# Kernel tuning notes

Measured on AMD Instinct MI355X. Metric: run time of the kernel, lower is better.

Reference implementation:

```python
import jax, jax.numpy as jnp
import numpy as np

N, E = 50000, 500000
IN_C, HID, OUT_C, HEADS, NL = 128, 16, 16, 8, 4
EPS = 1e-5
NEG_SLOPE = 0.2


def _gatv2(x, src, dst, Wl, Wr, att, bias, concat):
    # GATv2Conv (PyG semantics, eval mode): lin_l on source, lin_r on target,
    # e = a . LeakyReLU(xl[src] + xr[dst]); segment softmax over dst; scatter-sum.
    n = x.shape[0]
    H, C = att.shape
    xl = (x @ Wl).reshape(n, H, C)
    xr = (x @ Wr).reshape(n, H, C)
    e = jax.nn.leaky_relu(xl[src] + xr[dst], NEG_SLOPE)          # [E', H, C]
    logit = jnp.einsum('ehc,hc->eh', e, att)                      # [E', H]
    mx = jax.lax.stop_gradient(jax.ops.segment_max(logit, dst, num_segments=n))
    a = jnp.exp(logit - mx[dst])
    denom = jax.ops.segment_sum(a, dst, num_segments=n)
    alpha = a / denom[dst]                                        # [E', H]
    out = jax.ops.segment_sum(xl[src] * alpha[..., None], dst, num_segments=n)
    out = out.reshape(n, H * C) if concat else out.mean(axis=1)
    return out + bias


def _bn_eval(x, g, b, m, v):
    return (x - m) * jax.lax.rsqrt(v + EPS) * g + b


def setup_inputs() -> dict:
    key = jax.random.key(0)
    ks = jax.random.split(key, 32)
    d = {}
    d['x'] = jax.random.normal(ks[0], (N, IN_C), dtype=jnp.float32)
    d['edge_index'] = jax.random.randint(ks[1], (2, E), 0, N, dtype=jnp.int64)
    HC = HID * HEADS  # 128
    dims_in = [IN_C, HC, HC, HC]
    dims_h = [HEADS, HEADS, HEADS, 1]
    dims_c = [HID, HID, HID, OUT_C]
    ki = 2
    for i in range(NL):
        fan = dims_in[i]
        s = 1.0 / np.sqrt(fan)
        d[f'W{i}l'] = jax.random.uniform(ks[ki], (fan, dims_h[i] * dims_c[i]), minval=-s, maxval=s, dtype=jnp.float32); ki += 1
        d[f'W{i}r'] = jax.random.uniform(ks[ki], (fan, dims_h[i] * dims_c[i]), minval=-s, maxval=s, dtype=jnp.float32); ki += 1
        d[f'a{i}'] = jax.random.normal(ks[ki], (dims_h[i], dims_c[i]), dtype=jnp.float32) * 0.1; ki += 1
        out_dim = dims_h[i] * dims_c[i] if i < NL - 1 else dims_c[i]
        d[f'b{i}'] = jnp.zeros((out_dim,), dtype=jnp.float32)
    for i in range(NL - 1):
        d[f'g{i}'] = jnp.ones((HC,), dtype=jnp.float32) + 0.1 * jax.random.normal(ks[ki], (HC,), dtype=jnp.float32); ki += 1
        d[f'be{i}'] = 0.1 * jax.random.normal(ks[ki], (HC,), dtype=jnp.float32); ki += 1
        d[f'm{i}'] = 0.1 * jax.random.normal(ks[ki], (HC,), dtype=jnp.float32); ki += 1
        d[f'v{i}'] = jnp.ones((HC,), dtype=jnp.float32)
    return d


def reference(x, edge_index, W0l, W0r, a0, b0, W1l, W1r, a1, b1, W2l, W2r, a2, b2, W3l, W3r, a3, b3, g0, be0, m0, v0, g1, be1, m1, v1, g2, be2, m2, v2):
    n = x.shape[0]
    loop = jnp.arange(n, dtype=edge_index.dtype)
    src = jnp.concatenate([edge_index[0], loop])  # add_self_loops=True (PyG default)
    dst = jnp.concatenate([edge_index[1], loop])
    Ws = [(W0l, W0r, a0, b0), (W1l, W1r, a1, b1), (W2l, W2r, a2, b2), (W3l, W3r, a3, b3)]
    bns = [(g0, be0, m0, v0), (g1, be1, m1, v1), (g2, be2, m2, v2)]
    h = x
    for i in range(NL):
        Wl, Wr, att, bias = Ws[i]
        h = _gatv2(h, src, dst, Wl, Wr, att, bias, concat=(i < NL - 1))
        if i < NL - 1:
            g, b, m, v = bns[i]
            h = jax.nn.elu(_bn_eval(h, g, b, m, v))
    return h
```

## Files before the change

kernel.cpp:

```cpp
#include <hip/hip_runtime.h>
#include <hip/hip_fp16.h>
#include <math.h>

static constexpr float BN_EPS = 1e-5f;
static constexpr float NEG = 0.2f;

typedef float f32x4 __attribute__((ext_vector_type(4)));
typedef _Float16 h16x2 __attribute__((ext_vector_type(2)));
typedef _Float16 h16x8 __attribute__((ext_vector_type(8)));


__global__ __launch_bounds__(256) void hist_pack(
    const int* __restrict__ ei, int E, int n, int* __restrict__ cnt,
    const float* __restrict__ W0l, const float* __restrict__ W0r,
    const float* __restrict__ W1l, const float* __restrict__ W1r,
    const float* __restrict__ W2l, const float* __restrict__ W2r,
    const float* __restrict__ W3l, const float* __restrict__ W3r,
    __half* __restrict__ pk0, __half* __restrict__ pk1,
    __half* __restrict__ pk2, __half* __restrict__ pk3,
    const float* __restrict__ b0, const float* __restrict__ b1,
    const float* __restrict__ b2,
    const float* __restrict__ g0, const float* __restrict__ g1,
    const float* __restrict__ g2,
    const float* __restrict__ be0, const float* __restrict__ be1,
    const float* __restrict__ be2,
    const float* __restrict__ m0, const float* __restrict__ m1,
    const float* __restrict__ m2,
    const float* __restrict__ v0, const float* __restrict__ v1,
    const float* __restrict__ v2,
    float* __restrict__ bnA, float* __restrict__ bnB) {
    int b = blockIdx.x;
    if (b < 200) {
        if (threadIdx.x >= 64) return;
        const float *Wl, *Wr;
        __half* packed;
        int tile, NTT, M;
        if (b < 192) {
            int layer = b >> 6;
            tile = b & 63;
            NTT = 16; M = 128;
            Wl = (layer == 0) ? W0l : (layer == 1) ? W1l : W2l;
            Wr = (layer == 0) ? W0r : (layer == 1) ? W1r : W2r;
            packed = (layer == 0) ? pk0 : (layer == 1) ? pk1 : pk2;
        } else {
            tile = b - 192;
            NTT = 2; M = 16;
            Wl = W3l; Wr = W3r; packed = pk3;
        }
        int NT = NTT >> 1;
        int gnt = tile % NTT;
        int kt = tile / NTT;
        int l = threadIdx.x;
        const float* W = (gnt < NT) ? Wl : Wr;
        int col = (gnt % NT) * 16 + (l & 15);
        int krow = kt * 32 + ((l >> 4) << 3);
        size_t base = (size_t)tile * 512 + (size_t)l * 8;
#pragma unroll
        for (int j = 0; j < 8; j++)
            packed[base + j] = __float2half(W[(size_t)(krow + j) * M + col]);
    } else if (b == 200) {
        for (int t = threadIdx.x; t < 384; t += 256) {
            int layer = t >> 7;
            int c = t & 127;
            const float* gg = (layer == 0) ? g0 : (layer == 1) ? g1 : g2;
            const float* ee = (layer == 0) ? be0 : (layer == 1) ? be1 : be2;
            const float* mm = (layer == 0) ? m0 : (layer == 1) ? m1 : m2;
            const float* vv = (layer == 0) ? v0 : (layer == 1) ? v1 : v2;
            const float* bb = (layer == 0) ? b0 : (layer == 1) ? b1 : b2;
            float A = gg[c] * rsqrtf(vv[c] + BN_EPS);
            bnA[t] = A;
            bnB[t] = fmaf(bb[c] - mm[c], A, ee[c]);
        }
    } else {
        int e = (b - 201) * 256 + threadIdx.x;
        int ET = E + n;
        if (e >= ET) return;
        int d = (e < E) ? ei[E + e] : (e - E);
        atomicAdd(&cnt[d], 1);
    }
}


__device__ __forceinline__ void scan_block_body256(
    const int* __restrict__ cnt, int* __restrict__ rowptr,
    int* __restrict__ bsums, int n, int bid, int* s) {
    int t = threadIdx.x;
    int base = bid * 1024 + t * 4;
    int v0 = 0, v1 = 0, v2 = 0, v3 = 0;
    if (base + 3 < n) {
        v0 = cnt[base];     v1 = cnt[base + 1];
        v2 = cnt[base + 2]; v3 = cnt[base + 3];
    } else {
        if (base < n)     v0 = cnt[base];
        if (base + 1 < n) v1 = cnt[base + 1];
        if (base + 2 < n) v2 = cnt[base + 2];
        if (base + 3 < n) v3 = cnt[base + 3];
    }
    int p1 = v0 + v1, p2 = p1 + v2, p3 = p2 + v3;
    s[t] = p3;
    __syncthreads();
    for (int d = 1; d < 256; d <<= 1) {
        int tt = (t >= d) ? s[t - d] : 0;
        __syncthreads();
        s[t] += tt;
        __syncthreads();
    }
    int ex = s[t] - p3;
    if (base < n)     rowptr[base + 1] = ex + v0;
    if (base + 1 < n) rowptr[base + 2] = ex + p1;
    if (base + 2 < n) rowptr[base + 3] = ex + p2;
    if (base + 3 < n) rowptr[base + 4] = ex + p3;
    if (t == 255) bsums[bid] = s[255];
}

__global__ __launch_bounds__(1024) void scan_add2(
    int* __restrict__ rowptr, const int* __restrict__ bsums, int n, int nb) {
    __shared__ int sex;
    if (threadIdx.x < 64) {
        int L = threadIdx.x;
        int v = (L < nb) ? bsums[L] : 0;
#pragma unroll
        for (int d = 1; d < 64; d <<= 1) {
            int t = __shfl_up(v, d);
            if (L >= d) v += t;
        }
        int ex = __shfl_up(v, 1);
        if (L == 0) ex = 0;
        if (L == (int)blockIdx.x) sex = ex;
    }
    __syncthreads();
    int i = blockIdx.x * 1024 + threadIdx.x;
    if (i < n) rowptr[i + 1] += sex;
    if (i == 0) rowptr[0] = 0;
}

__global__ void scatter_kernel(const int* __restrict__ ei, int E, int n,
                               const int* __restrict__ rowptr, int* __restrict__ fill,
                               int* __restrict__ col) {
    int e = blockIdx.x * blockDim.x + threadIdx.x;
    int ET = E + n;
    if (e >= ET) return;
    int s, d;
    if (e < E) { s = ei[e]; d = ei[E + e]; } else { s = e - E; d = s; }
    int pos = atomicAdd(&fill[d], 1);
    col[rowptr[d] + pos] = s;
}


template <bool FIRST>
__device__ __forceinline__ void gemm_body(
    const __half* __restrict__ xh, const float* __restrict__ xf,
    const __half* __restrict__ packed,
    __half* __restrict__ Y1, __half* __restrict__ Y2, int n, int bid,
    _Float16* sA) {
    const int t = threadIdx.x;
    const int row0 = bid * 64;

    for (int c = t; c < 1024; c += 256) {
        int row = c >> 4;
        int off = (c & 15) * 8;
        int gr = row0 + row;
        if (gr >= n) gr = n - 1;
        if (FIRST) {
            float4 v0 = *(const float4*)&xf[(size_t)gr * 128 + off];
            float4 v1 = *(const float4*)&xf[(size_t)gr * 128 + off + 4];
            h16x8 h = {(_Float16)v0.x, (_Float16)v0.y, (_Float16)v0.z, (_Float16)v0.w,
                       (_Float16)v1.x, (_Float16)v1.y, (_Float16)v1.z, (_Float16)v1.w};
            *(h16x8*)&sA[row * 136 + off] = h;
        } else {
            *(h16x8*)&sA[row * 136 + off] = *(const h16x8*)&xh[(size_t)gr * 128 + off];
        }
    }
    __syncthreads();

    const int lane = t & 63;
    const int s = t >> 6;
    const int lr = lane & 15;
    const int kq = (lane >> 4) * 8;

    h16x8 af[4][4];
#pragma unroll
    for (int rt = 0; rt < 4; rt++)
#pragma unroll
        for (int kt = 0; kt < 4; kt++)
            af[rt][kt] = *(const h16x8*)&sA[(rt * 16 + lr) * 136 + kt * 32 + kq];

    f32x4 acc[4][4];
#pragma unroll
    for (int a = 0; a < 4; a++)
#pragma unroll
        for (int b = 0; b < 4; b++) acc[a][b] = (f32x4){0.f, 0.f, 0.f, 0.f};

#pragma unroll
    for (int kt = 0; kt < 4; kt++) {
#pragma unroll
        for (int ntl = 0; ntl < 4; ntl++) {
            int nt = s * 4 + ntl;
            h16x8 b = *(const h16x8*)&packed[((size_t)(kt * 16 + nt)) * 512 + lane * 8];
#pragma unroll
            for (int rt = 0; rt < 4; rt++)
                acc[ntl][rt] = __builtin_amdgcn_mfma_f32_16x16x32_f16(af[rt][kt], b, acc[ntl][rt], 0, 0, 0);
        }
    }

    __half* Y = (s < 2) ? Y1 : Y2;
    const int colh = (s & 1) * 64;
    const int rq = (lane >> 4) * 4;
#pragma unroll
    for (int ntl = 0; ntl < 4; ntl++) {
        int col = colh + ntl * 16 + lr;
#pragma unroll
        for (int rt = 0; rt < 4; rt++) {
#pragma unroll
            for (int g = 0; g < 4; g++) {
                int row = row0 + rt * 16 + rq + g;
                if (row < n) Y[(size_t)row * 128 + col] = __float2half(acc[ntl][rt][g]);
            }
        }
    }
}

__global__ __launch_bounds__(256) void gemm_h_big2(
    const __half* __restrict__ xh, const __half* __restrict__ packed,
    __half* __restrict__ Y1, __half* __restrict__ Y2, int n) {
    __shared__ __align__(16) char smem[64 * 136 * 2];
    gemm_body<false>(xh, nullptr, packed, Y1, Y2, n, blockIdx.x, (_Float16*)smem);
}

__global__ __launch_bounds__(256) void scanblk_gemm0(
    const int* __restrict__ cnt, int* __restrict__ rowptr,
    int* __restrict__ bsums, int n, int nscan,
    const float* __restrict__ xf, const __half* __restrict__ packed,
    __half* __restrict__ Y1, __half* __restrict__ Y2) {
    __shared__ __align__(16) char smem[64 * 136 * 2];
    int b = blockIdx.x;
    if (b < nscan) {
        scan_block_body256(cnt, rowptr, bsums, n, b, (int*)smem);
    } else {
        gemm_body<true>(nullptr, xf, packed, Y1, Y2, n, b - nscan,
                        (_Float16*)smem);
    }
}


__global__ __launch_bounds__(256) void gemm_h_small(
    const __half* __restrict__ xh, const __half* __restrict__ packed,
    float* __restrict__ Y1, float* __restrict__ Y2, int n) {
    int lane = threadIdx.x & 63;
    int wv = blockIdx.x * 4 + (threadIdx.x >> 6);
    int row0 = wv * 16;
    if (row0 >= n) return;
    int r = row0 + (lane & 15);
    if (r >= n) r = n - 1;
    int kq = (lane >> 4) * 8;

    h16x8 af[4];
#pragma unroll
    for (int kt = 0; kt < 4; kt++)
        af[kt] = *(const h16x8*)&xh[(size_t)r * 128 + kt * 32 + kq];

    f32x4 acc[2];
    acc[0] = (f32x4){0.f, 0.f, 0.f, 0.f};
    acc[1] = (f32x4){0.f, 0.f, 0.f, 0.f};

#pragma unroll
    for (int kt = 0; kt < 4; kt++) {
#pragma unroll
        for (int nt = 0; nt < 2; nt++) {
            h16x8 b = *(const h16x8*)&packed[((size_t)(kt * 2 + nt)) * 512 + lane * 8];
            acc[nt] = __builtin_amdgcn_mfma_f32_16x16x32_f16(af[kt], b, acc[nt], 0, 0, 0);
        }
    }

    int colb = lane & 15;
    int rbase = row0 + (lane >> 4) * 4;
#pragma unroll
    for (int nt = 0; nt < 2; nt++) {
        float* Y = (nt == 0) ? Y1 : Y2;
#pragma unroll
        for (int g = 0; g < 4; g++) {
            int row = rbase + g;
            if (row < n) Y[(size_t)row * 16 + colb] = acc[nt][g];
        }
    }
}


__device__ __forceinline__ float dot8_h(const h16x2* lp, const h16x2* ap) {
#if __has_builtin(__builtin_amdgcn_fdot2)
    float part = __builtin_amdgcn_fdot2(lp[0], ap[0], 0.f, false);
    part = __builtin_amdgcn_fdot2(lp[1], ap[1], part, false);
    part = __builtin_amdgcn_fdot2(lp[2], ap[2], part, false);
    return __builtin_amdgcn_fdot2(lp[3], ap[3], part, false);
#else
    float part = 0.f;
#pragma unroll
    for (int i = 0; i < 4; i++)
        part += (float)lp[i].x * (float)ap[i].x + (float)lp[i].y * (float)ap[i].y;
    return part;
#endif
}

__global__ __launch_bounds__(256) void agg_h(
    const __half* __restrict__ xl, const __half* __restrict__ xr,
    const int* __restrict__ rowptr, const int* __restrict__ col,
    const float* __restrict__ att,
    const float* __restrict__ bnA, const float* __restrict__ bnB,
    __half* __restrict__ oh, int n) {
    int v = (blockIdx.x * blockDim.x + threadIdx.x) >> 4;
    if (v >= n) return;
    int L = threadIdx.x & 15;
    int ch = L * 8;

    int beg = rowptr[v];
    int end = rowptr[v + 1];
    int cb = beg;
    int cidx = (cb + L < end) ? col[cb + L] : v;

    h16x8 rx = *(const h16x8*)&xr[((size_t)v << 7) + ch];
    float4 av0 = *(const float4*)&att[ch];
    float4 av1 = *(const float4*)&att[ch + 4];
    h16x2 a[4] = {{(_Float16)av0.x, (_Float16)av0.y},
                  {(_Float16)av0.z, (_Float16)av0.w},
                  {(_Float16)av1.x, (_Float16)av1.y},
                  {(_Float16)av1.z, (_Float16)av1.w}};
    const h16x8 neg8 = {(_Float16)NEG, (_Float16)NEG, (_Float16)NEG, (_Float16)NEG,
                        (_Float16)NEG, (_Float16)NEG, (_Float16)NEG, (_Float16)NEG};

    float lrun = 0.f;
    float acc[8] = {0.f, 0.f, 0.f, 0.f, 0.f, 0.f, 0.f, 0.f};

    auto proc = [&](h16x8 hv, bool ok) {
        h16x8 s = hv + rx;
        h16x8 l = __builtin_elementwise_max(s, s * neg8);
        const h16x2* lp = (const h16x2*)&l;
        float part = dot8_h(lp, a);
        part += __shfl_xor(part, 1);
        float p = ok ? __expf(part) : 0.f;
        lrun += p;
        const _Float16* hp = (const _Float16*)&hv;
#pragma unroll
        for (int k = 0; k < 8; k++) acc[k] = fmaf(p, (float)hp[k], acc[k]);
    };

    while (true) {
        int ce = min(end, cb + 16);
        for (int e = cb; e < ce; e += 4) {
            int off = e - cb;
            h16x8 hv[4];
#pragma unroll
            for (int j = 0; j < 4; j++) {
                int u = __shfl(cidx, off + j, 16);
                hv[j] = *(const h16x8*)&xl[((size_t)u << 7) + ch];
            }
#pragma unroll
            for (int j = 0; j < 4; j++) proc(hv[j], e + j < end);
        }
        cb += 16;
        if (cb >= end) break;
        cidx = (cb + L < end) ? col[cb + L] : v;
    }

    float inv = 1.0f / lrun;
    float4 A0 = *(const float4*)&bnA[ch];
    float4 A1 = *(const float4*)&bnA[ch + 4];
    float4 B0 = *(const float4*)&bnB[ch];
    float4 B1 = *(const float4*)&bnB[ch + 4];
    float Av[8] = {A0.x, A0.y, A0.z, A0.w, A1.x, A1.y, A1.z, A1.w};
    float Bv[8] = {B0.x, B0.y, B0.z, B0.w, B1.x, B1.y, B1.z, B1.w};
    h16x8 outv;
#pragma unroll
    for (int k = 0; k < 8; k++) {
        float o = fmaf(acc[k], inv * Av[k], Bv[k]);
        o = o > 0.f ? o : expm1f(o);
        outv[k] = (_Float16)o;
    }
    *(h16x8*)&oh[((size_t)v << 7) + ch] = outv;
}


__global__ __launch_bounds__(256) void agg_f(
    const float* __restrict__ xl, const float* __restrict__ xr,
    const int* __restrict__ rowptr, const int* __restrict__ col,
    const float* __restrict__ att, const float* __restrict__ bias,
    float* __restrict__ out, int n) {
    int v = (blockIdx.x * blockDim.x + threadIdx.x) >> 2;
    if (v >= n) return;
    int L = threadIdx.x & 3;
    int ch = 4 * L;

    int beg = rowptr[v];
    int end = rowptr[v + 1];
    int cb = beg;
    int cidx = (cb + L < end) ? col[cb + L] : v;

    float4 xrv = *(const float4*)&xr[((size_t)v << 4) + ch];
    float4 av = *(const float4*)&att[ch];

    float lrun = 0.f;
    float4 acc = make_float4(0.f, 0.f, 0.f, 0.f);

    while (true) {
        float4 xv[4];
#pragma unroll
        for (int j = 0; j < 4; j++) {
            int u = __shfl(cidx, j, 4);
            xv[j] = *(const float4*)&xl[((size_t)u << 4) + ch];
        }
#pragma unroll
        for (int j = 0; j < 4; j++) {
            bool ok = (cb + j < end);
            float s0 = xv[j].x + xrv.x; s0 = s0 > 0.f ? s0 : NEG * s0;
            float s1 = xv[j].y + xrv.y; s1 = s1 > 0.f ? s1 : NEG * s1;
            float s2 = xv[j].z + xrv.z; s2 = s2 > 0.f ? s2 : NEG * s2;
            float s3 = xv[j].w + xrv.w; s3 = s3 > 0.f ? s3 : NEG * s3;
            float part = fmaf(s0, av.x, fmaf(s1, av.y, fmaf(s2, av.z, s3 * av.w)));
            part += __shfl_xor(part, 1);
            part += __shfl_xor(part, 2);
            float p = ok ? __expf(part) : 0.f;
            lrun += p;
            acc.x = fmaf(p, xv[j].x, acc.x);
            acc.y = fmaf(p, xv[j].y, acc.y);
            acc.z = fmaf(p, xv[j].z, acc.z);
            acc.w = fmaf(p, xv[j].w, acc.w);
        }
        cb += 4;
        if (cb >= end) break;
        cidx = (cb + L < end) ? col[cb + L] : v;
    }

    float inv = 1.0f / lrun;
    float4 b4 = *(const float4*)&bias[ch];
    *(float4*)&out[((size_t)v << 4) + ch] =
        make_float4(fmaf(acc.x, inv, b4.x), fmaf(acc.y, inv, b4.y),
                    fmaf(acc.z, inv, b4.z), fmaf(acc.w, inv, b4.w));
}


extern "C" void kernel_launch(void* const* d_in, const int* in_sizes, int n_in,
                              void* d_out, int out_size, void* d_ws, size_t ws_size,
                              hipStream_t stream) {
    const float* x = (const float*)d_in[0];
    const int* ei = (const int*)d_in[1];
    const float* Wl[4] = {(const float*)d_in[2], (const float*)d_in[6],
                          (const float*)d_in[10], (const float*)d_in[14]};
    const float* Wr[4] = {(const float*)d_in[3], (const float*)d_in[7],
                          (const float*)d_in[11], (const float*)d_in[15]};
    const float* att[4] = {(const float*)d_in[4], (const float*)d_in[8],
                           (const float*)d_in[12], (const float*)d_in[16]};
    const float* bias[4] = {(const float*)d_in[5], (const float*)d_in[9],
                            (const float*)d_in[13], (const float*)d_in[17]};
    const float* g[3] = {(const float*)d_in[18], (const float*)d_in[22], (const float*)d_in[26]};
    const float* be[3] = {(const float*)d_in[19], (const float*)d_in[23], (const float*)d_in[27]};
    const float* bm[3] = {(const float*)d_in[20], (const float*)d_in[24], (const float*)d_in[28]};
    const float* bv[3] = {(const float*)d_in[21], (const float*)d_in[25], (const float*)d_in[29]};

    const int n = in_sizes[0] / 128;
    const int E = in_sizes[1] / 2;
    const int ET = E + n;

    char* p = (char*)d_ws;
    __half* xh = (__half*)p;           p += (size_t)n * 128 * 2;
    __half* xlh = (__half*)p;          p += (size_t)n * 128 * 2;
    __half* xrh = (__half*)p;          p += (size_t)n * 128 * 2;
    float* xl3 = (float*)p;            p += (size_t)n * 16 * 4;
    float* xr3 = (float*)p;            p += (size_t)n * 16 * 4;
    int* rowptr = (int*)p;            p += (size_t)(n + 4) * 4;
    int* cnt = (int*)p;               p += (size_t)n * 4;
    int* fill = (int*)p;              p += (size_t)n * 4;
    int* col = (int*)p;               p += (size_t)ET * 4;
    int* bsums = (int*)p;             p += 256;
    __half* pk[4];
    for (int i = 0; i < 3; i++) { pk[i] = (__half*)p; p += 4 * 16 * 512 * 2; }
    pk[3] = (__half*)p;               p += 4 * 2 * 512 * 2;
    float* bnA = (float*)p;           p += 384 * 4;
    float* bnB = (float*)p;           p += 384 * 4;

    (void)hipMemsetAsync(cnt, 0, (size_t)n * 8, stream);

    const int tb = 256;
    const int histBlocks = (ET + tb - 1) / tb;
    hist_pack<<<201 + histBlocks, tb, 0, stream>>>(
        ei, E, n, cnt,
        Wl[0], Wr[0], Wl[1], Wr[1], Wl[2], Wr[2], Wl[3], Wr[3],
        pk[0], pk[1], pk[2], pk[3],
        bias[0], bias[1], bias[2],
        g[0], g[1], g[2], be[0], be[1], be[2],
        bm[0], bm[1], bm[2], bv[0], bv[1], bv[2],
        bnA, bnB);

    const int nb = (n + 1023) / 1024;
    const int gb64 = (n + 63) / 64;
    const int gemmBlocksSmall = ((n + 15) / 16 + 3) / 4;
    const int aggBlocksH = (n + 15) / 16;
    const int aggBlocksF = (n + 63) / 64;

    scanblk_gemm0<<<nb + gb64, 256, 0, stream>>>(
        cnt, rowptr, bsums, n, nb, x, pk[0], xlh, xrh);
    scan_add2<<<nb, 1024, 0, stream>>>(rowptr, bsums, n, nb);
    scatter_kernel<<<(ET + tb - 1) / tb, tb, 0, stream>>>(ei, E, n, rowptr, fill, col);

    agg_h<<<aggBlocksH, 256, 0, stream>>>(
        xlh, xrh, rowptr, col, att[0], bnA, bnB, xh, n);
    for (int i = 1; i < 3; i++) {
        gemm_h_big2<<<gb64, 256, 0, stream>>>(xh, pk[i], xlh, xrh, n);
        agg_h<<<aggBlocksH, 256, 0, stream>>>(
            xlh, xrh, rowptr, col, att[i], bnA + 128 * i, bnB + 128 * i, xh, n);
    }
    gemm_h_small<<<gemmBlocksSmall, 256, 0, stream>>>(xh, pk[3], xl3, xr3, n);
    agg_f<<<aggBlocksF, 256, 0, stream>>>(
        xl3, xr3, rowptr, col, att[3], bias[3], (float*)d_out, n);
}
```

Baseline: 329.6 us.

## Fuse scan finalize and scatter into gemm0 launch; widen agg_h lanes to 16 channels

Scan block-finalization and the CSR scatter now run inside the layer-0 GEMM launch, and each block recomputes the block-prefix offsets itself. The scan kernel is split out to run alone, and two small dependent launches are removed. agg_h now uses 8 lanes per node with 16 channels each, which covers a head with no cross-lane shuffle reduction. It also prefetches the next column chunk, so index loads overlap with compute. The trade-off is more registers per thread and fewer lanes per node, which could lower memory-level parallelism.

```diff
diff --git a/kernel.cpp b/kernel.cpp
--- a/kernel.cpp
+++ b/kernel.cpp
@@ -113,37 +113,11 @@
     if (t == 255) bsums[bid] = s[255];
 }
 
-__global__ __launch_bounds__(1024) void scan_add2(
-    int* __restrict__ rowptr, const int* __restrict__ bsums, int n, int nb) {
-    __shared__ int sex;
-    if (threadIdx.x < 64) {
-        int L = threadIdx.x;
-        int v = (L < nb) ? bsums[L] : 0;
-#pragma unroll
-        for (int d = 1; d < 64; d <<= 1) {
-            int t = __shfl_up(v, d);
-            if (L >= d) v += t;
-        }
-        int ex = __shfl_up(v, 1);
-        if (L == 0) ex = 0;
-        if (L == (int)blockIdx.x) sex = ex;
-    }
-    __syncthreads();
-    int i = blockIdx.x * 1024 + threadIdx.x;
-    if (i < n) rowptr[i + 1] += sex;
-    if (i == 0) rowptr[0] = 0;
-}
-
-__global__ void scatter_kernel(const int* __restrict__ ei, int E, int n,
-                               const int* __restrict__ rowptr, int* __restrict__ fill,
-                               int* __restrict__ col) {
-    int e = blockIdx.x * blockDim.x + threadIdx.x;
-    int ET = E + n;
-    if (e >= ET) return;
-    int s, d;
-    if (e < E) { s = ei[e]; d = ei[E + e]; } else { s = e - E; d = s; }
-    int pos = atomicAdd(&fill[d], 1);
-    col[rowptr[d] + pos] = s;
+__global__ __launch_bounds__(256) void scan_only(
+    const int* __restrict__ cnt, int* __restrict__ rowraw,
+    int* __restrict__ bsums, int n) {
+    __shared__ int s[256];
+    scan_block_body256(cnt, rowraw, bsums, n, blockIdx.x, s);
 }
 
 
@@ -227,18 +201,51 @@
     gemm_body<false>(xh, nullptr, packed, Y1, Y2, n, blockIdx.x, (_Float16*)smem);
 }
 
-__global__ __launch_bounds__(256) void scanblk_gemm0(
-    const int* __restrict__ cnt, int* __restrict__ rowptr,
-    int* __restrict__ bsums, int n, int nscan,
+
+__global__ __launch_bounds__(256) void scatfin_gemm0(
+    const int* __restrict__ ei, int E, int n,
+    const int* __restrict__ rowraw, const int* __restrict__ bsums, int nb,
+    int* __restrict__ fill, int* __restrict__ col, int* __restrict__ rowfin,
     const float* __restrict__ xf, const __half* __restrict__ packed,
-    __half* __restrict__ Y1, __half* __restrict__ Y2) {
+    __half* __restrict__ Y1, __half* __restrict__ Y2, int gb, int nbF) {
     __shared__ __align__(16) char smem[64 * 136 * 2];
     int b = blockIdx.x;
-    if (b < nscan) {
-        scan_block_body256(cnt, rowptr, bsums, n, b, (int*)smem);
+    if (b < gb) {
+        gemm_body<true>(nullptr, xf, packed, Y1, Y2, n, b, (_Float16*)smem);
+        return;
+    }
+    int* spre = (int*)smem;
+    if (threadIdx.x < 64) {
+        int L = threadIdx.x;
+        int bv = (L < nb) ? bsums[L] : 0;
+#pragma unroll
+        for (int d = 1; d < 64; d <<= 1) {
+            int t = __shfl_up(bv, d);
+            if (L >= d) bv += t;
+        }
+        int ex = __shfl_up(bv, 1);
+        if (L == 0) ex = 0;
+        spre[L] = ex;
+    }
+    __syncthreads();
+    b -= gb;
+    if (b < nbF) {
+        int i0 = b * 1024 + threadIdx.x * 4;
+#pragma unroll
+        for (int j = 0; j < 4; j++) {
+            int i = i0 + j;
+            if (i < n) rowfin[i + 1] = rowraw[i + 1] + spre[i >> 10];
+        }
+        if (b == 0 && threadIdx.x == 0) rowfin[0] = 0;
     } else {
-        gemm_body<true>(nullptr, xf, packed, Y1, Y2, n, b - nscan,
-                        (_Float16*)smem);
+        int e = (b - nbF) * 256 + threadIdx.x;
+        int ET = E + n;
+        if (e >= ET) return;
+        int s, d;
+        if (e < E) { s = ei[e]; d = ei[E + e]; } else { s = e - E; d = s; }
+        int pos = atomicAdd(&fill[d], 1);
+        int base = (d == 0) ? 0 : (rowraw[d] + spre[(d - 1) >> 10]);
+        col[base + pos] = s;
     }
 }
 
@@ -286,96 +293,126 @@
 }
 
 
-__device__ __forceinline__ float dot8_h(const h16x2* lp, const h16x2* ap) {
-#if __has_builtin(__builtin_amdgcn_fdot2)
-    float part = __builtin_amdgcn_fdot2(lp[0], ap[0], 0.f, false);
-    part = __builtin_amdgcn_fdot2(lp[1], ap[1], part, false);
-    part = __builtin_amdgcn_fdot2(lp[2], ap[2], part, false);
-    return __builtin_amdgcn_fdot2(lp[3], ap[3], part, false);
-#else
-    float part = 0.f;
-#pragma unroll
-    for (int i = 0; i < 4; i++)
-        part += (float)lp[i].x * (float)ap[i].x + (float)lp[i].y * (float)ap[i].y;
-    return part;
-#endif
-}
-
 __global__ __launch_bounds__(256) void agg_h(
     const __half* __restrict__ xl, const __half* __restrict__ xr,
     const int* __restrict__ rowptr, const int* __restrict__ col,
     const float* __restrict__ att,
     const float* __restrict__ bnA, const float* __restrict__ bnB,
     __half* __restrict__ oh, int n) {
-    int v = (blockIdx.x * blockDim.x + threadIdx.x) >> 4;
+    int v = (blockIdx.x * blockDim.x + threadIdx.x) >> 3;
     if (v >= n) return;
-    int L = threadIdx.x & 15;
-    int ch = L * 8;
+    int L = threadIdx.x & 7;
+    int ch = L * 16;
 
     int beg = rowptr[v];
     int end = rowptr[v + 1];
     int cb = beg;
     int cidx = (cb + L < end) ? col[cb + L] : v;
 
-    h16x8 rx = *(const h16x8*)&xr[((size_t)v << 7) + ch];
-    float4 av0 = *(const float4*)&att[ch];
-    float4 av1 = *(const float4*)&att[ch + 4];
-    h16x2 a[4] = {{(_Float16)av0.x, (_Float16)av0.y},
-                  {(_Float16)av0.z, (_Float16)av0.w},
-                  {(_Float16)av1.x, (_Float16)av1.y},
-                  {(_Float16)av1.z, (_Float16)av1.w}};
+    const __half* xrb = &xr[((size_t)v << 7) + ch];
+    h16x8 rx0 = *(const h16x8*)xrb;
+    h16x8 rx1 = *(const h16x8*)(xrb + 8);
+    float4 af0 = *(const float4*)&att[ch];
+    float4 af1 = *(const float4*)&att[ch + 4];
+    float4 af2 = *(const float4*)&att[ch + 8];
+    float4 af3 = *(const float4*)&att[ch + 12];
+    h16x2 a[8] = {{(_Float16)af0.x, (_Float16)af0.y}, {(_Float16)af0.z, (_Float16)af0.w},
+                  {(_Float16)af1.x, (_Float16)af1.y}, {(_Float16)af1.z, (_Float16)af1.w},
+                  {(_Float16)af2.x, (_Float16)af2.y}, {(_Float16)af2.z, (_Float16)af2.w},
+                  {(_Float16)af3.x, (_Float16)af3.y}, {(_Float16)af3.z, (_Float16)af3.w}};
     const h16x8 neg8 = {(_Float16)NEG, (_Float16)NEG, (_Float16)NEG, (_Float16)NEG,
                         (_Float16)NEG, (_Float16)NEG, (_Float16)NEG, (_Float16)NEG};
 
     float lrun = 0.f;
-    float acc[8] = {0.f, 0.f, 0.f, 0.f, 0.f, 0.f, 0.f, 0.f};
-
-    auto proc = [&](h16x8 hv, bool ok) {
-        h16x8 s = hv + rx;
-        h16x8 l = __builtin_elementwise_max(s, s * neg8);
-        const h16x2* lp = (const h16x2*)&l;
-        float part = dot8_h(lp, a);
-        part += __shfl_xor(part, 1);
-        float p = ok ? __expf(part) : 0.f;
-        lrun += p;
-        const _Float16* hp = (const _Float16*)&hv;
-#pragma unroll
-        for (int k = 0; k < 8; k++) acc[k] = fmaf(p, (float)hp[k], acc[k]);
-    };
+    float acc[16];
+#pragma unroll
+    for (int k = 0; k < 16; k++) acc[k] = 0.f;
 
     while (true) {
-        int ce = min(end, cb + 16);
+        int nxtb = cb + 8;
+        bool more = (nxtb < end);
+        int cidx_n = v;
+        if (more && (nxtb + L < end)) cidx_n = col[nxtb + L];
+        int ce = min(end, nxtb);
         for (int e = cb; e < ce; e += 4) {
             int off = e - cb;
-            h16x8 hv[4];
+            h16x8 hv0[4], hv1[4];
 #pragma unroll
             for (int j = 0; j < 4; j++) {
-                int u = __shfl(cidx, off + j, 16);
-                hv[j] = *(const h16x8*)&xl[((size_t)u << 7) + ch];
+                int u = __shfl(cidx, off + j, 8);
+                const __half* s = &xl[((size_t)u << 7) + ch];
+                hv0[j] = *(const h16x8*)s;
+                hv1[j] = *(const h16x8*)(s + 8);
             }
 #pragma unroll
-            for (int j = 0; j < 4; j++) proc(hv[j], e + j < end);
-        }
-        cb += 16;
-        if (cb >= end) break;
-        cidx = (cb + L < end) ? col[cb + L] : v;
+            for (int j = 0; j < 4; j++) {
+                bool ok = (e + j < end);
+                h16x8 s0 = hv0[j] + rx0;
+                h16x8 s1 = hv1[j] + rx1;
+                h16x8 l0 = __builtin_elementwise_max(s0, s0 * neg8);
+                h16x8 l1 = __builtin_elementwise_max(s1, s1 * neg8);
+                const h16x2* l0p = (const h16x2*)&l0;
+                const h16x2* l1p = (const h16x2*)&l1;
+#if __has_builtin(__builtin_amdgcn_fdot2)
+                float part = __builtin_amdgcn_fdot2(l0p[0], a[0], 0.f, false);
+                part = __builtin_amdgcn_fdot2(l0p[1], a[1], part, false);
+                part = __builtin_amdgcn_fdot2(l0p[2], a[2], part, false);
+                part = __builtin_amdgcn_fdot2(l0p[3], a[3], part, false);
+                part = __builtin_amdgcn_fdot2(l1p[0], a[4], part, false);
+                part = __builtin_amdgcn_fdot2(l1p[1], a[5], part, false);
+                part = __builtin_amdgcn_fdot2(l1p[2], a[6], part, false);
+                part = __builtin_amdgcn_fdot2(l1p[3], a[7], part, false);
+#else
+                float part = 0.f;
+#pragma unroll
+                for (int i = 0; i < 4; i++)
+                    part += (float)l0p[i].x * (float)a[i].x + (float)l0p[i].y * (float)a[i].y
+                          + (float)l1p[i].x * (float)a[4 + i].x + (float)l1p[i].y * (float)a[4 + i].y;
+#endif
+                float p = ok ? __expf(part) : 0.f;
+                lrun += p;
+                const _Float16* h0 = (const _Float16*)&hv0[j];
+                const _Float16* h1 = (const _Float16*)&hv1[j];
+#pragma unroll
+                for (int k = 0; k < 8; k++) acc[k] = fmaf(p, (float)h0[k], acc[k]);
+#pragma unroll
+                for (int k = 0; k < 8; k++) acc[8 + k] = fmaf(p, (float)h1[k], acc[8 + k]);
+            }
+        }
+        if (!more) break;
+        cb = nxtb;
+        cidx = cidx_n;
     }
 
     float inv = 1.0f / lrun;
     float4 A0 = *(const float4*)&bnA[ch];
     float4 A1 = *(const float4*)&bnA[ch + 4];
+    float4 A2 = *(const float4*)&bnA[ch + 8];
+    float4 A3 = *(const float4*)&bnA[ch + 12];
     float4 B0 = *(const float4*)&bnB[ch];
     float4 B1 = *(const float4*)&bnB[ch + 4];
-    float Av[8] = {A0.x, A0.y, A0.z, A0.w, A1.x, A1.y, A1.z, A1.w};
-    float Bv[8] = {B0.x, B0.y, B0.z, B0.w, B1.x, B1.y, B1.z, B1.w};
-    h16x8 outv;
+    float4 B2 = *(const float4*)&bnB[ch + 8];
+    float4 B3 = *(const float4*)&bnB[ch + 12];
+    float Av[16] = {A0.x, A0.y, A0.z, A0.w, A1.x, A1.y, A1.z, A1.w,
+                    A2.x, A2.y, A2.z, A2.w, A3.x, A3.y, A3.z, A3.w};
+    float Bv[16] = {B0.x, B0.y, B0.z, B0.w, B1.x, B1.y, B1.z, B1.w,
+                    B2.x, B2.y, B2.z, B2.w, B3.x, B3.y, B3.z, B3.w};
+    h16x8 o0, o1;
 #pragma unroll
     for (int k = 0; k < 8; k++) {
         float o = fmaf(acc[k], inv * Av[k], Bv[k]);
         o = o > 0.f ? o : expm1f(o);
-        outv[k] = (_Float16)o;
-    }
-    *(h16x8*)&oh[((size_t)v << 7) + ch] = outv;
+        o0[k] = (_Float16)o;
+    }
+#pragma unroll
+    for (int k = 0; k < 8; k++) {
+        float o = fmaf(acc[8 + k], inv * Av[8 + k], Bv[8 + k]);
+        o = o > 0.f ? o : expm1f(o);
+        o1[k] = (_Float16)o;
+    }
+    __half* ob = &oh[((size_t)v << 7) + ch];
+    *(h16x8*)ob = o0;
+    *(h16x8*)(ob + 8) = o1;
 }
 
 
@@ -465,7 +502,8 @@
     __half* xrh = (__half*)p;          p += (size_t)n * 128 * 2;
     float* xl3 = (float*)p;            p += (size_t)n * 16 * 4;
     float* xr3 = (float*)p;            p += (size_t)n * 16 * 4;
-    int* rowptr = (int*)p;            p += (size_t)(n + 4) * 4;
+    int* rowraw = (int*)p;            p += (size_t)(n + 4) * 4;
+    int* rowfin = (int*)p;            p += (size_t)(n + 4) * 4;
     int* cnt = (int*)p;               p += (size_t)n * 4;
     int* fill = (int*)p;              p += (size_t)n * 4;
     int* col = (int*)p;               p += (size_t)ET * 4;
@@ -492,22 +530,23 @@
     const int nb = (n + 1023) / 1024;
     const int gb64 = (n + 63) / 64;
     const int gemmBlocksSmall = ((n + 15) / 16 + 3) / 4;
-    const int aggBlocksH = (n + 15) / 16;
+    const int aggBlocksH = (n + 31) / 32;
     const int aggBlocksF = (n + 63) / 64;
 
-    scanblk_gemm0<<<nb + gb64, 256, 0, stream>>>(
-        cnt, rowptr, bsums, n, nb, x, pk[0], xlh, xrh);
-    scan_add2<<<nb, 1024, 0, stream>>>(rowptr, bsums, n, nb);
-    scatter_kernel<<<(ET + tb - 1) / tb, tb, 0, stream>>>(ei, E, n, rowptr, fill, col);
+    scan_only<<<nb, 256, 0, stream>>>(cnt, rowraw, bsums, n);
+
+    scatfin_gemm0<<<gb64 + nb + histBlocks, 256, 0, stream>>>(
+        ei, E, n, rowraw, bsums, nb, fill, col, rowfin,
+        x, pk[0], xlh, xrh, gb64, nb);
 
     agg_h<<<aggBlocksH, 256, 0, stream>>>(
-        xlh, xrh, rowptr, col, att[0], bnA, bnB, xh, n);
+        xlh, xrh, rowfin, col, att[0], bnA, bnB, xh, n);
     for (int i = 1; i < 3; i++) {
         gemm_h_big2<<<gb64, 256, 0, stream>>>(xh, pk[i], xlh, xrh, n);
         agg_h<<<aggBlocksH, 256, 0, stream>>>(
-            xlh, xrh, rowptr, col, att[i], bnA + 128 * i, bnB + 128 * i, xh, n);
+            xlh, xrh, rowfin, col, att[i], bnA + 128 * i, bnB + 128 * i, xh, n);
     }
     gemm_h_small<<<gemmBlocksSmall, 256, 0, stream>>>(xh, pk[3], xl3, xr3, n);
     agg_f<<<aggBlocksF, 256, 0, stream>>>(
-        xl3, xr3, rowptr, col, att[3], bias[3], (float*)d_out, n);
-}
+        xl3, xr3, rowfin, col, att[3], bias[3], (float*)d_out, n);
+}
```

Result: slower. 336.8 us (+2.2%).
